# Kernel optimization log

Hardware: AMD Instinct MI355X
Metric: run time of the kernel (lower is better)

Reference implementation:

```python
import jax, jax.numpy as jnp
import numpy as np
from jax import lax

D_MODEL = 384
D_INNER = 768          # expand * d_model
D_HALF = D_INNER // 2  # 384
D_STATE = 16
D_CONV = 4
DT_RANK = 24           # ceil(384/16)
BATCH = 8
SEQLEN = 4097
EXTRAS = 1
LMAIN = SEQLEN - EXTRAS


def setup_inputs() -> dict:
    key = jax.random.key(0)
    ks = jax.random.split(key, 12)
    hidden_states = jax.random.normal(ks[0], (BATCH, SEQLEN, D_MODEL), jnp.float32)
    in_proj_w = jax.random.normal(ks[1], (D_INNER, D_MODEL), jnp.float32) * 0.02
    conv_x_w = jax.random.normal(ks[2], (D_HALF, 1, D_CONV), jnp.float32) * 0.2
    conv_z_w = jax.random.normal(ks[3], (D_HALF, 1, D_CONV), jnp.float32) * 0.2
    x_proj_w = jax.random.normal(ks[4], (DT_RANK + 2 * D_STATE, D_HALF), jnp.float32) * 0.02
    dt_std = DT_RANK ** -0.5
    dt_proj_w = jax.random.uniform(ks[5], (D_HALF, DT_RANK), jnp.float32, -dt_std, dt_std)
    # bias = inverse softplus of dt sampled log-uniform in [1e-3, 1e-1]
    dt = jnp.exp(jax.random.uniform(ks[6], (D_HALF,), jnp.float32)
                 * (jnp.log(0.1) - jnp.log(0.001)) + jnp.log(0.001))
    dt = jnp.clip(dt, 1e-4, None)
    dt_proj_b = dt + jnp.log(-jnp.expm1(-dt))
    A_log = jnp.log(jnp.broadcast_to(jnp.arange(1, D_STATE + 1, dtype=jnp.float32),
                                     (D_HALF, D_STATE)))
    D_param = jnp.ones((D_HALF,), jnp.float32)
    out_proj_w = jax.random.normal(ks[7], (D_MODEL, D_HALF), jnp.float32) * 0.02
    perm = jax.random.permutation(ks[8], LMAIN).astype(jnp.int64)
    perm_rev = jnp.argsort(perm).astype(jnp.int64)
    return {
        "hidden_states": hidden_states,
        "in_proj_w": in_proj_w,
        "conv_x_w": conv_x_w,
        "conv_z_w": conv_z_w,
        "x_proj_w": x_proj_w,
        "dt_proj_w": dt_proj_w,
        "dt_proj_b": dt_proj_b,
        "A_log": A_log,
        "D_param": D_param,
        "out_proj_w": out_proj_w,
        "perm": perm,
        "perm_rev": perm_rev,
    }


def _depthwise_conv_same(x, w):
    # x: (B, C, L), w: (C, 1, K); torch padding='same' for k=4 -> pad (left=1, right=2)
    total = D_CONV - 1
    left = total // 2
    return lax.conv_general_dilated(
        x, w, window_strides=(1,), padding=[(left, total - left)],
        dimension_numbers=("NCH", "OIH", "NCH"), feature_group_count=D_HALF)


def _selective_scan(x, dt, A, Bm, Cm, D_param, delta_bias):
    # x, dt: (B, d, L); A: (d, n); Bm, Cm: (B, n, L)
    dt = jax.nn.softplus(dt + delta_bias[None, :, None])
    xT = jnp.moveaxis(x, 2, 0)    # (L, B, d)
    dtT = jnp.moveaxis(dt, 2, 0)  # (L, B, d)
    BT = jnp.moveaxis(Bm, 2, 0)   # (L, B, n)
    CT = jnp.moveaxis(Cm, 2, 0)   # (L, B, n)

    def step(h, inp):
        x_t, dt_t, B_t, C_t = inp
        dA = jnp.exp(dt_t[..., None] * A)                      # (B, d, n)
        h = h * dA + (dt_t * x_t)[..., None] * B_t[:, None, :]  # (B, d, n)
        y = jnp.einsum("bdn,bn->bd", h, C_t)
        return h, y

    h0 = jnp.zeros((x.shape[0], x.shape[1], A.shape[1]), x.dtype)
    _, ys = lax.scan(step, h0, (xT, dtT, BT, CT))
    y = jnp.moveaxis(ys, 0, 2)  # (B, d, L)
    return y + D_param[None, :, None] * x


def reference(hidden_states, in_proj_w, conv_x_w, conv_z_w, x_proj_w,
              dt_proj_w, dt_proj_b, A_log, D_param, out_proj_w, perm, perm_rev):
    # in_proj (no bias): (B,L,D) -> (B, d_inner, L)
    xz = jnp.einsum("bld,ed->bel", hidden_states, in_proj_w)
    # hilbert/zigzag reorder on the main (non-extra) tokens
    xz = jnp.concatenate([xz[:, :, :EXTRAS], xz[:, :, EXTRAS:][:, :, perm]], axis=2)

    x, z = jnp.split(xz, 2, axis=1)  # (B, d_half, L) each
    A = -jnp.exp(A_log)
    x = jax.nn.silu(_depthwise_conv_same(x, conv_x_w))
    z = jax.nn.silu(_depthwise_conv_same(z, conv_z_w))

    x_dbl = jnp.einsum("bdl,ed->bel", x, x_proj_w)  # (B, dt_rank+2n, L)
    dt_low, Bm, Cm = jnp.split(x_dbl, [DT_RANK, DT_RANK + D_STATE], axis=1)
    dt = jnp.einsum("brl,dr->bdl", dt_low, dt_proj_w)

    y = _selective_scan(x, dt, A, Bm, Cm, D_param, dt_proj_b)
    y = (y * z).transpose(0, 2, 1)  # (B, L, d_half)
    out = jnp.einsum("bld,ed->ble", y, out_proj_w)  # (B, L, D)
    # undo the permutation on the output
    out = jnp.concatenate([out[:, :EXTRAS], out[:, EXTRAS:][:, perm_rev]], axis=1)
    return out
```

## Files before the change

kernel.cpp:

```cpp
#include <hip/hip_runtime.h>
#include <hip/hip_bf16.h>

#define DEVI __device__ __forceinline__

constexpr int B_   = 8;
constexpr int L_   = 4097;
constexpr int MTOT = B_ * L_;
constexpr int DH   = 384;
constexpr int NS   = 16;
constexpr int CH   = 33;
constexpr int NCH  = (L_ + CH - 1) / CH;

typedef __bf16 bf16x8 __attribute__((ext_vector_type(8)));
typedef float  f32x4  __attribute__((ext_vector_type(4)));

DEVI float bl(unsigned v) { return __uint_as_float(v << 16); }
DEVI float bh(unsigned v) { return __uint_as_float(v & 0xffff0000u); }
DEVI float bf(const __hip_bfloat16 x) { return __bfloat162float(x); }
DEVI unsigned short f2bu(float x) {
  __hip_bfloat16 b = __float2bfloat16(x);
  return *(unsigned short*)&b;
}
DEVI float u16f(const uint4& u, int j) {
  const unsigned w = (&u.x)[j >> 1];
  return (j & 1) ? bh(w) : bl(w);
}
DEVI float softplus_f(float x) {
  return (x > 20.f) ? x : __logf(1.f + __expf(x));
}

DEVI void gld16(const __hip_bfloat16* g, __hip_bfloat16* l) {
  __builtin_amdgcn_global_load_lds(
      (const __attribute__((address_space(1))) void*)g,
      (__attribute__((address_space(3))) void*)l, 16, 0, 0);
}

__global__ void flag_k(const void* hs, int* flagp) {
  if (threadIdx.x == 0 && blockIdx.x == 0) {
    const unsigned short* u = (const unsigned short*)hs;
    int ok = 1;
    for (int i = 0; i < 8; ++i) {
      const unsigned short v = u[2 * i];
      const int e = (v >> 7) & 0xFF;
      if (!(v == 0 || (e >= 100 && e <= 140))) ok = 0;
    }
    flagp[0] = ok;
    flagp[1] = 1;
  }
}

__global__ void a2prep_k(const void* __restrict__ alog, float* __restrict__ a2fo,
                         int* flagp) {
  const int d = threadIdx.x;
  const int f = flagp[0];
  float a2[16];
#pragma unroll
  for (int n = 0; n < 16; ++n) {
    const float v = f ? bf(((const __hip_bfloat16*)alog)[d * 16 + n])
                      : ((const float*)alog)[d * 16 + n];
    a2[n] = -1.4426950408889634f * __expf(v);
    a2fo[d * 16 + n] = a2[n];
  }
  int ok = 1;
#pragma unroll
  for (int n = 1; n < 16; ++n) {
    const float ref = (float)(n + 1) * a2[0];
    if (fabsf(a2[n] - ref) > 1e-3f * fabsf(ref)) ok = 0;
  }
  if (!ok) atomicAnd(&flagp[1], 0);
}

__global__ void perm_k(const int* p0, const int* p1, int* d0, int* d1) {
  __shared__ int s_or;
  const int* src = blockIdx.x ? p1 : p0;
  int*       dst = blockIdx.x ? d1 : d0;
  if (threadIdx.x == 0) s_or = 0;
  __syncthreads();
  int loc = 0;
  for (int i = threadIdx.x; i < 2048; i += 1024) loc |= src[2 * i + 1];
  atomicOr(&s_or, loc);
  __syncthreads();
  const bool is64 = (s_or == 0);
  for (int j = threadIdx.x; j < 4096; j += 1024)
    dst[j] = is64 ? (int)((const long long*)src)[j] : src[j];
}

struct NormSet { const void* src[8]; void* dst[8]; int n[8]; };
__global__ void norm_all(NormSet s, const int* flagp) {
  const int idx = blockIdx.x * 256 + threadIdx.x;
  const int f = flagp[0];
#pragma unroll
  for (int t = 0; t < 8; ++t) {
    if (idx < s.n[t]) {
      __hip_bfloat16* d = (__hip_bfloat16*)s.dst[t];
      if (f) d[idx] = ((const __hip_bfloat16*)s.src[t])[idx];
      else   d[idx] = __float2bfloat16(((const float*)s.src[t])[idx]);
    }
  }
}

__global__ void prep_k(const __hip_bfloat16* __restrict__ dtw,
                       const __hip_bfloat16* __restrict__ xw,
                       __hip_bfloat16* __restrict__ wcomb) {
  const int idx = blockIdx.x * 256 + threadIdx.x;
  if (idx >= 512 * 384) return;
  const int n = idx / 384, k = idx - n * 384;
  float v = 0.f;
  if (n < 384) {
#pragma unroll
    for (int r = 0; r < 24; ++r) v += bf(dtw[n * 24 + r]) * bf(xw[r * 384 + k]);
  } else if (n < 416) {
    v = bf(xw[(24 + n - 384) * 384 + k]);
  }
  wcomb[idx] = __float2bfloat16(v);
}

__global__ void cvt_k(const void* __restrict__ hs, __hip_bfloat16* __restrict__ dst,
                      const int* __restrict__ gidx, const int* __restrict__ flagp) {
  const int idx = blockIdx.x * 256 + threadIdx.x;
  if (idx >= MTOT * 48) return;
  const int j = idx % 48;
  const int r = idx / 48;
  const int b = r / L_, t = r - b * L_;
  const int src = b * L_ + (t == 0 ? 0 : 1 + gidx[t - 1]);
  uint4 o;
  if (flagp[0]) {
    o = *(const uint4*)((const __hip_bfloat16*)hs + (size_t)src * 384 + j * 8);
  } else {
    const float* f = (const float*)hs + (size_t)src * 384 + j * 8;
    const float4 f0 = *(const float4*)f;
    const float4 f1 = *(const float4*)(f + 4);
    o.x = f2bu(f0.x) | ((unsigned)f2bu(f0.y) << 16);
    o.y = f2bu(f0.z) | ((unsigned)f2bu(f0.w) << 16);
    o.z = f2bu(f1.x) | ((unsigned)f2bu(f1.y) << 16);
    o.w = f2bu(f1.z) | ((unsigned)f2bu(f1.w) << 16);
  }
  *(uint4*)(dst + (size_t)r * 384 + j * 8) = o;
}

template<int GATHER, int EPI>
__global__ __launch_bounds__(256, 3)
void gemm_k(const __hip_bfloat16* __restrict__ A, const __hip_bfloat16* __restrict__ W,
            void* __restrict__ e0, void* __restrict__ e1,
            const __hip_bfloat16* __restrict__ bias,
            const int* __restrict__ gidx, const int* __restrict__ flagp,
            int M, int N)
{
  __shared__ __align__(16) char smem[36864];
  __hip_bfloat16* lA = (__hip_bfloat16*)smem;
  __hip_bfloat16* lB = lA + 2 * 128 * 32;
  const int tid  = threadIdx.x;
  const int lane = tid & 63;
  const int wv   = tid >> 6;
  const int wm   = wv >> 1, wn = wv & 1;
  const int lrow = lane & 15, quad = lane >> 4;
  const int fbf  = flagp[0];

  const int NT = gridDim.x;
  const int nblocks = NT * (int)gridDim.y;
  const int id = blockIdx.y * NT + blockIdx.x;
  const int q8 = nblocks >> 3, r8 = nblocks & 7;
  const int xcd = id & 7, slot = id >> 3;
  const int nid = (xcd < r8 ? xcd * (q8 + 1)
                            : r8 * (q8 + 1) + (xcd - r8) * q8) + slot;
  const int mt = nid / NT, nt = nid - mt * NT;

  const bool live = !(EPI == 1 && nt * 128 + wn * 64 >= 416);

  const __hip_bfloat16* aSrc[4];
  const __hip_bfloat16* bSrc[4];
  __hip_bfloat16* aDst[4];
  __hip_bfloat16* bDst[4];
#pragma unroll
  for (int p = 0; p < 4; ++p) {
    const int s   = p * 256 + tid;
    const int kh  = s >> 9;
    const int row = (s >> 2) & 127;
    const int kc  = kh * 32 + (s & 3) * 8;
    int r = mt * 128 + row;
    if (r >= M) r = M - 1;
    int src;
    if (GATHER) { const int b = r / L_, t = r - b * L_;
                  src = b * L_ + (t == 0 ? 0 : 1 + gidx[t - 1]); }
    else        { src = r; }
    aSrc[p] = A + (size_t)src * 384 + kc;
    bSrc[p] = W + (size_t)(nt * 128 + row) * 384 + kc;
    aDst[p] = &lA[s * 8];
    bDst[p] = &lB[s * 8];
  }

  f32x4 acc[4][4] = {};

#pragma unroll
  for (int kt = 0; kt < 6; ++kt) {
    __syncthreads();
#pragma unroll
    for (int p = 0; p < 4; ++p) gld16(aSrc[p] + kt * 64, aDst[p]);
#pragma unroll
    for (int p = 0; p < 4; ++p) gld16(bSrc[p] + kt * 64, bDst[p]);
    __syncthreads();
    if (live) {
#pragma unroll
      for (int kh = 0; kh < 2; ++kh) {
        bf16x8 af[4], bfr[4];
#pragma unroll
        for (int i = 0; i < 4; ++i)
          af[i] = *reinterpret_cast<const bf16x8*>(
              &lA[kh * 4096 + (wm * 64 + i * 16 + lrow) * 32 + quad * 8]);
#pragma unroll
        for (int j = 0; j < 4; ++j)
          bfr[j] = *reinterpret_cast<const bf16x8*>(
              &lB[kh * 4096 + (wn * 64 + j * 16 + lrow) * 32 + quad * 8]);
#pragma unroll
        for (int i = 0; i < 4; ++i)
#pragma unroll
          for (int j = 0; j < 4; ++j)
            acc[i][j] = __builtin_amdgcn_mfma_f32_16x16x32_bf16(af[i], bfr[j], acc[i][j], 0, 0, 0);
      }
    }
  }

  const int r0c = mt * 128;
  if (EPI == 1 && nt == 3) {
#pragma unroll
    for (int i = 0; i < 4; ++i) {
      const int row0 = r0c + wm * 64 + i * 16 + quad * 4;
#pragma unroll
      for (int j = 0; j < 4; ++j) {
        const int col = 384 + wn * 64 + j * 16 + lrow;
        if (col >= 416) continue;
#pragma unroll
        for (int rg = 0; rg < 4; ++rg) {
          const int r = row0 + rg;
          if (r >= M) continue;
          ((float*)e1)[(size_t)r * 32 + (col - 384)] = acc[i][j][rg];
        }
      }
    }
  } else if (EPI == 2 && !fbf) {
    float* lT = (float*)smem;
#pragma unroll
    for (int h = 0; h < 2; ++h) {
      __syncthreads();
      if (wn == h) {
#pragma unroll
        for (int i = 0; i < 4; ++i)
#pragma unroll
          for (int j = 0; j < 4; ++j)
#pragma unroll
            for (int rg = 0; rg < 4; ++rg)
              lT[(wm * 64 + i * 16 + quad * 4 + rg) * 72 + j * 16 + lrow] = acc[i][j][rg];
      }
      __syncthreads();
#pragma unroll
      for (int p = 0; p < 8; ++p) {
        const int ch = p * 256 + tid;
        const int row = ch >> 4, c4 = (ch & 15) * 4;
        const int r = r0c + row;
        if (r < M) {
          const float4 v = *(const float4*)&lT[row * 72 + c4];
          *(float4*)((float*)e0 + (size_t)r * 384 + nt * 128 + h * 64 + c4) = v;
        }
      }
    }
  } else {
    __hip_bfloat16* lT = (__hip_bfloat16*)smem;
#pragma unroll
    for (int h = 0; h < 2; ++h) {
      __syncthreads();
      if (wn == h) {
        float bj[4] = {};
        if (EPI == 1) {
#pragma unroll
          for (int j = 0; j < 4; ++j)
            bj[j] = bf(bias[nt * 128 + h * 64 + j * 16 + lrow]);
        }
#pragma unroll
        for (int i = 0; i < 4; ++i)
#pragma unroll
          for (int j = 0; j < 4; ++j)
#pragma unroll
            for (int rg = 0; rg < 4; ++rg) {
              float v = acc[i][j][rg];
              if (EPI == 1) v = softplus_f(v + bj[j]);
              lT[(wm * 64 + i * 16 + quad * 4 + rg) * 72 + j * 16 + lrow] =
                  __float2bfloat16(v);
            }
      }
      __syncthreads();
#pragma unroll
      for (int p = 0; p < 4; ++p) {
        const int ch = p * 256 + tid;
        const int row = ch >> 3, c8 = (ch & 7) * 8;
        const int r = r0c + row;
        if (r < M) {
          const uint4 v = *(const uint4*)&lT[row * 72 + c8];
          const int g = nt * 128 + h * 64 + c8;
          __hip_bfloat16* dst = (EPI == 0 && g >= 384)
                ? (__hip_bfloat16*)e1 + (size_t)r * 384 + (g - 384)
                : (__hip_bfloat16*)e0 + (size_t)r * 384 + g;
          *(uint4*)dst = v;
        }
      }
    }
  }
}

__global__ void convx_k(const __hip_bfloat16* __restrict__ xh,
                        const __hip_bfloat16* __restrict__ cxw,
                        __hip_bfloat16* __restrict__ xc) {
  const int idx = blockIdx.x * 256 + threadIdx.x;
  if (idx >= MTOT * 48) return;
  const int g  = idx % 48;
  const int rg = idx / 48;
  const int t  = rg % L_;
  const int c0 = g * 8;
  uint4 wv[4];
#pragma unroll
  for (int p = 0; p < 4; ++p) wv[p] = *(const uint4*)(cxw + c0 * 4 + p * 8);
  float acc[8] = {};
#pragma unroll
  for (int k = 0; k < 4; ++k) {
    const int tt = t + k - 1;
    if (tt < 0 || tt >= L_) continue;
    const uint4 u = *(const uint4*)(xh + (size_t)(rg + k - 1) * 384 + c0);
#pragma unroll
    for (int j = 0; j < 8; ++j) {
      const int e = j * 4 + k;
      acc[j] += u16f(wv[e >> 3], e & 7) * u16f(u, j);
    }
  }
  uint4 o;
#pragma unroll
  for (int p = 0; p < 4; ++p) {
    const float s0 = acc[2 * p]     / (1.f + __expf(-acc[2 * p]));
    const float s1 = acc[2 * p + 1] / (1.f + __expf(-acc[2 * p + 1]));
    (&o.x)[p] = f2bu(s0) | ((unsigned)f2bu(s1) << 16);
  }
  *(uint4*)(xc + (size_t)rg * 384 + c0) = o;
}

__global__ __launch_bounds__(128)
void scan1_k(const __hip_bfloat16* __restrict__ dt, const float* __restrict__ bc,
             __hip_bfloat16* xcio,
             const float* __restrict__ a2f,
             const __hip_bfloat16* __restrict__ dpar,
             float* __restrict__ pbuf, float* __restrict__ hend,
             const int* __restrict__ flagp)
{
  __shared__ __align__(16) float lBC[CH * 32];
  const int blk = blockIdx.x;
  const int dt3 = blk % 3;
  const int c   = (blk / 3) % NCH;
  const int b   = blk / (3 * NCH);
  const int d   = dt3 * 128 + threadIdx.x;
  const int t0  = c * CH;
  const int r0  = b * L_ + t0;
  const int tmax = (L_ - t0 < CH) ? (L_ - t0) : CH;
  for (int i = threadIdx.x; i < tmax * 32; i += 128) lBC[i] = bc[(size_t)r0 * 32 + i];
  __syncthreads();

  float h[16];
#pragma unroll
  for (int n = 0; n < 16; ++n) h[n] = 0.f;
  float sdt = 0.f;
  const float Dd = bf(dpar[d]);
  const size_t base = ((size_t)(c * 8 + b) * 16) * 384 + d;

  if (flagp[1]) {
    const float a2b = a2f[d * 16];
    for (int tt = 0; tt < tmax; ++tt) {
      const size_t r = (size_t)(r0 + tt);
      const float dtv = bf(dt[r * 384 + d]);
      const float xv  = bf(xcio[r * 384 + d]);
      sdt += dtv;
      const float dtx = dtv * xv;
      float pw[17];
      pw[1] = exp2f(dtv * a2b);
#pragma unroll
      for (int n = 2; n <= 16; ++n) pw[n] = pw[n >> 1] * pw[n - (n >> 1)];
      float4 bq[4], cq[4];
#pragma unroll
      for (int q = 0; q < 4; ++q) {
        bq[q] = *(const float4*)&lBC[tt * 32 + q * 4];
        cq[q] = *(const float4*)&lBC[tt * 32 + 16 + q * 4];
      }
      float ya = 0.f, yb = 0.f;
#pragma unroll
      for (int n = 0; n < 16; ++n) {
        h[n] = h[n] * pw[n + 1] + dtx * (&bq[n >> 2].x)[n & 3];
        const float t = h[n] * (&cq[n >> 2].x)[n & 3];
        if (n & 1) yb += t; else ya += t;
      }
      const float y = ya + yb + Dd * xv;
      xcio[r * 384 + d] = __float2bfloat16(y);
    }
    float Ep[17];
    Ep[1] = exp2f(sdt * a2b);
#pragma unroll
    for (int n = 2; n <= 16; ++n) Ep[n] = Ep[n >> 1] * Ep[n - (n >> 1)];
#pragma unroll
    for (int n = 0; n < 16; ++n) {
      pbuf[base + n * 384] = Ep[n + 1];
      hend[base + n * 384] = h[n];
    }
  } else {
    float a2[16];
#pragma unroll
    for (int n = 0; n < 16; ++n) a2[n] = a2f[d * 16 + n];
    for (int tt = 0; tt < tmax; ++tt) {
      const size_t r = (size_t)(r0 + tt);
      const float dtv = bf(dt[r * 384 + d]);
      const float xv  = bf(xcio[r * 384 + d]);
      sdt += dtv;
      const float dtx = dtv * xv;
      float4 bq[4], cq[4];
#pragma unroll
      for (int q = 0; q < 4; ++q) {
        bq[q] = *(const float4*)&lBC[tt * 32 + q * 4];
        cq[q] = *(const float4*)&lBC[tt * 32 + 16 + q * 4];
      }
      float ya = 0.f, yb = 0.f;
#pragma unroll
      for (int n = 0; n < 16; ++n) {
        h[n] = h[n] * exp2f(dtv * a2[n]) + dtx * (&bq[n >> 2].x)[n & 3];
        const float t = h[n] * (&cq[n >> 2].x)[n & 3];
        if (n & 1) yb += t; else ya += t;
      }
      const float y = ya + yb + Dd * xv;
      xcio[r * 384 + d] = __float2bfloat16(y);
    }
#pragma unroll
    for (int n = 0; n < 16; ++n) {
      pbuf[base + n * 384] = exp2f(sdt * a2[n]);
      hend[base + n * 384] = h[n];
    }
  }
}

__global__ void scan2_k(float* __restrict__ pbuf, const float* __restrict__ hend) {
  const int tid = blockIdx.x * 256 + threadIdx.x;
  const int d = tid % 384;
  const int n = (tid / 384) & 15;
  const int b = tid / 6144;
  float H = 0.f;
  for (int c = 0; c < NCH; ++c) {
    const size_t idx = ((size_t)(c * 8 + b) * 16 + n) * 384 + d;
    const float p = pbuf[idx];
    const float he = hend[idx];
    pbuf[idx] = H;
    H = p * H + he;
  }
}

__global__ __launch_bounds__(128)
void scan3_k(__hip_bfloat16* dtyg, const float* __restrict__ bc,
             const __hip_bfloat16* __restrict__ yl,
             const __hip_bfloat16* __restrict__ zh,
             const __hip_bfloat16* __restrict__ czw,
             const float* __restrict__ a2f,
             const float* __restrict__ hstart,
             const int* __restrict__ flagp)
{
  __shared__ __align__(16) float lC[CH * 16];
  const int blk = blockIdx.x;
  const int dt3 = blk % 3;
  const int c   = (blk / 3) % NCH;
  const int b   = blk / (3 * NCH);
  const int d   = dt3 * 128 + threadIdx.x;
  const int t0  = c * CH;
  const int r0  = b * L_ + t0;
  const int tmax = (L_ - t0 < CH) ? (L_ - t0) : CH;
  for (int i = threadIdx.x; i < tmax * 16; i += 128)
    lC[i] = bc[(size_t)r0 * 32 + (i >> 4) * 32 + 16 + (i & 15)];
  __syncthreads();

  float hs_[16];
  const size_t base = ((size_t)(c * 8 + b) * 16) * 384 + d;
#pragma unroll
  for (int n = 0; n < 16; ++n) hs_[n] = hstart[base + n * 384];
  float cw[4];
#pragma unroll
  for (int k = 0; k < 4; ++k) cw[k] = bf(czw[d * 4 + k]);

  float zm1 = (t0 - 1 >= 0) ? bf(zh[(size_t)(r0 - 1) * 384 + d]) : 0.f;
  float z0  = bf(zh[(size_t)r0 * 384 + d]);
  float zp1 = (t0 + 1 < L_) ? bf(zh[(size_t)(r0 + 1) * 384 + d]) : 0.f;
  float sdt = 0.f;

  if (flagp[1]) {
    const float a2b = a2f[d * 16];
    for (int tt = 0; tt < tmax; ++tt) {
      const int t = t0 + tt;
      const size_t r = (size_t)(r0 + tt);
      const float zp2 = (t + 2 < L_) ? bf(zh[(r + 2) * 384 + d]) : 0.f;
      const float dtv = bf(dtyg[r * 384 + d]);
      sdt += dtv;
      float pw[17];
      pw[1] = exp2f(sdt * a2b);
#pragma unroll
      for (int n = 2; n <= 16; ++n) pw[n] = pw[n >> 1] * pw[n - (n >> 1)];
      float4 cq[4];
#pragma unroll
      for (int q = 0; q < 4; ++q) cq[q] = *(const float4*)&lC[tt * 16 + q * 4];
      float ca = 0.f, cb = 0.f;
#pragma unroll
      for (int n = 0; n < 16; ++n) {
        const float t2 = (&cq[n >> 2].x)[n & 3] * hs_[n] * pw[n + 1];
        if (n & 1) cb += t2; else ca += t2;
      }
      const float y = bf(yl[r * 384 + d]) + ca + cb;
      const float zc = cw[0] * zm1 + cw[1] * z0 + cw[2] * zp1 + cw[3] * zp2;
      const float zs = zc / (1.f + __expf(-zc));
      dtyg[r * 384 + d] = __float2bfloat16(y * zs);
      zm1 = z0; z0 = zp1; zp1 = zp2;
    }
  } else {
    float a2[16];
#pragma unroll
    for (int n = 0; n < 16; ++n) a2[n] = a2f[d * 16 + n];
    for (int tt = 0; tt < tmax; ++tt) {
      const int t = t0 + tt;
      const size_t r = (size_t)(r0 + tt);
      const float zp2 = (t + 2 < L_) ? bf(zh[(r + 2) * 384 + d]) : 0.f;
      const float dtv = bf(dtyg[r * 384 + d]);
      sdt += dtv;
      float4 cq[4];
#pragma unroll
      for (int q = 0; q < 4; ++q) cq[q] = *(const float4*)&lC[tt * 16 + q * 4];
      float ca = 0.f, cb = 0.f;
#pragma unroll
      for (int n = 0; n < 16; ++n) {
        const float t2 = (&cq[n >> 2].x)[n & 3] * hs_[n] * exp2f(sdt * a2[n]);
        if (n & 1) cb += t2; else ca += t2;
      }
      const float y = bf(yl[r * 384 + d]) + ca + cb;
      const float zc = cw[0] * zm1 + cw[1] * z0 + cw[2] * zp1 + cw[3] * zp2;
      const float zs = zc / (1.f + __expf(-zc));
      dtyg[r * 384 + d] = __float2bfloat16(y * zs);
      zm1 = z0; z0 = zp1; zp1 = zp2;
    }
  }
}

extern "C" void kernel_launch(void* const* d_in, const int* in_sizes, int n_in,
                              void* d_out, int out_size, void* d_ws, size_t ws_size,
                              hipStream_t stream) {
  const void* hs   = d_in[0];
  const void* w_in = d_in[1];
  const void* cxw  = d_in[2];
  const void* czw  = d_in[3];
  const void* xw   = d_in[4];
  const void* dtw  = d_in[5];
  const void* dtb  = d_in[6];
  const void* alog = d_in[7];
  const void* dpar = d_in[8];
  const void* ow   = d_in[9];
  const int* perm  = (const int*)d_in[10];
  const int* permr = (const int*)d_in[11];

  char* ws = (char*)d_ws;
  size_t off = 0;
  auto alloc = [&](size_t nbytes) -> char* {
    char* p = ws + off;
    off += (nbytes + 255) & ~(size_t)255;
    return p;
  };
  int* flag              = (int*)alloc(256);
  int* nperm             = (int*)alloc(4096 * 4);
  int* npermr            = (int*)alloc(4096 * 4);
  float* a2f             = (float*)alloc(6144 * 4);
  __hip_bfloat16* w_inb  = (__hip_bfloat16*)alloc(294912 * 2);
  __hip_bfloat16* cxwb   = (__hip_bfloat16*)alloc(1536 * 2);
  __hip_bfloat16* czwb   = (__hip_bfloat16*)alloc(1536 * 2);
  __hip_bfloat16* xwb    = (__hip_bfloat16*)alloc(21504 * 2);
  __hip_bfloat16* dtwb   = (__hip_bfloat16*)alloc(9216 * 2);
  __hip_bfloat16* dtbb   = (__hip_bfloat16*)alloc(384 * 2);
  __hip_bfloat16* dparb  = (__hip_bfloat16*)alloc(384 * 2);
  __hip_bfloat16* owb    = (__hip_bfloat16*)alloc(147456 * 2);
  __hip_bfloat16* wcombb = (__hip_bfloat16*)alloc((size_t)512 * 384 * 2);
  __hip_bfloat16* hsb    = (__hip_bfloat16*)alloc((size_t)MTOT * 384 * 2);
  __hip_bfloat16* zh     = (__hip_bfloat16*)alloc((size_t)MTOT * 384 * 2);
  __hip_bfloat16* xc     = (__hip_bfloat16*)alloc((size_t)MTOT * 384 * 2);
  __hip_bfloat16* dtyg   = (__hip_bfloat16*)alloc((size_t)MTOT * 384 * 2);
  float*          bcf    = (float*)alloc((size_t)MTOT * 32 * 4);
  __hip_bfloat16* xh   = (__hip_bfloat16*)d_out;
  float*          pbuf = (float*)d_out;
  float*          hend = (float*)((char*)d_out + (size_t)NCH * B_ * NS * DH * 4);

  flag_k<<<1, 64, 0, stream>>>(hs, flag);
  perm_k<<<2, 1024, 0, stream>>>(perm, permr, nperm, npermr);
  a2prep_k<<<1, 384, 0, stream>>>(alog, a2f, flag);
  NormSet ns;
  ns.src[0] = w_in; ns.dst[0] = w_inb; ns.n[0] = 294912;
  ns.src[1] = ow;   ns.dst[1] = owb;   ns.n[1] = 147456;
  ns.src[2] = xw;   ns.dst[2] = xwb;   ns.n[2] = 21504;
  ns.src[3] = dtw;  ns.dst[3] = dtwb;  ns.n[3] = 9216;
  ns.src[4] = cxw;  ns.dst[4] = cxwb;  ns.n[4] = 1536;
  ns.src[5] = czw;  ns.dst[5] = czwb;  ns.n[5] = 1536;
  ns.src[6] = dtb;  ns.dst[6] = dtbb;  ns.n[6] = 384;
  ns.src[7] = dpar; ns.dst[7] = dparb; ns.n[7] = 384;
  norm_all<<<1152, 256, 0, stream>>>(ns, flag);
  prep_k<<<768, 256, 0, stream>>>(dtwb, xwb, wcombb);
  cvt_k<<<(MTOT * 48 + 255) / 256, 256, 0, stream>>>(hs, hsb, nperm, flag);
  gemm_k<0, 0><<<dim3(6, 257), 256, 0, stream>>>(
      hsb, w_inb, xh, zh, nullptr, nullptr, flag, MTOT, 768);
  convx_k<<<(MTOT * 48 + 255) / 256, 256, 0, stream>>>(xh, cxwb, xc);
  gemm_k<0, 1><<<dim3(4, 257), 256, 0, stream>>>(
      xc, wcombb, dtyg, bcf, dtbb, nullptr, flag, MTOT, 512);
  scan1_k<<<B_ * NCH * 3, 128, 0, stream>>>(dtyg, bcf, xc, a2f, dparb, pbuf, hend, flag);
  scan2_k<<<192, 256, 0, stream>>>(pbuf, hend);
  scan3_k<<<B_ * NCH * 3, 128, 0, stream>>>(dtyg, bcf, xc, zh, czwb, a2f, pbuf, flag);
  gemm_k<1, 2><<<dim3(3, 257), 256, 0, stream>>>(
      dtyg, owb, d_out, nullptr, nullptr, npermr, flag, MTOT, 384);
  (void)in_sizes; (void)n_in; (void)out_size; (void)ws_size;
}
```

Before: 330.6 us.

## Restructure chunked scan: state-only first pass, recompute full recurrence from carried-in state

The first scan pass now only advances the hidden state over each chunk and stores the chunk's summed dt, no longer computing or writing per-token y. The prefix pass rebuilds each chunk's decay factor from the summed dt and A on the fly. The third pass reruns the full recurrence from the correct starting state, fusing the output and gating in one place. This removes the per-token y write and re-read and the stored decay buffer, at the cost of running the recurrence twice. Chunk size drops from 33 to 22, which gives more blocks but a longer sequential prefix pass.

```diff
diff --git a/kernel.cpp b/kernel.cpp
--- a/kernel.cpp
+++ b/kernel.cpp
@@ -8,7 +8,7 @@
 constexpr int MTOT = B_ * L_;
 constexpr int DH   = 384;
 constexpr int NS   = 16;
-constexpr int CH   = 33;
+constexpr int CH   = 22;
 constexpr int NCH  = (L_ + CH - 1) / CH;
 
 typedef __bf16 bf16x8 __attribute__((ext_vector_type(8)));
@@ -342,10 +342,98 @@
 
 __global__ __launch_bounds__(128)
 void scan1_k(const __hip_bfloat16* __restrict__ dt, const float* __restrict__ bc,
-             __hip_bfloat16* xcio,
+             const __hip_bfloat16* __restrict__ xc,
              const float* __restrict__ a2f,
+             float* __restrict__ sdtc, float* __restrict__ hend,
+             const int* __restrict__ flagp)
+{
+  __shared__ __align__(16) float lB[CH * 16];
+  const int blk = blockIdx.x;
+  const int dt3 = blk % 3;
+  const int c   = (blk / 3) % NCH;
+  const int b   = blk / (3 * NCH);
+  const int d   = dt3 * 128 + threadIdx.x;
+  const int t0  = c * CH;
+  const int r0  = b * L_ + t0;
+  const int tmax = (L_ - t0 < CH) ? (L_ - t0) : CH;
+  for (int i = threadIdx.x; i < tmax * 16; i += 128)
+    lB[i] = bc[(size_t)r0 * 32 + (i >> 4) * 32 + (i & 15)];
+  __syncthreads();
+
+  float h[16];
+#pragma unroll
+  for (int n = 0; n < 16; ++n) h[n] = 0.f;
+  float sdt = 0.f;
+  const size_t hbase = ((size_t)(c * 8 + b) * 16) * 384 + d;
+
+  if (flagp[1]) {
+    const float a2b = a2f[d * 16];
+    for (int tt = 0; tt < tmax; ++tt) {
+      const size_t r = (size_t)(r0 + tt);
+      const float dtv = bf(dt[r * 384 + d]);
+      const float xv  = bf(xc[r * 384 + d]);
+      sdt += dtv;
+      const float dtx = dtv * xv;
+      float pw[17];
+      pw[1] = exp2f(dtv * a2b);
+#pragma unroll
+      for (int n = 2; n <= 16; ++n) pw[n] = pw[n >> 1] * pw[n - (n >> 1)];
+      float4 bq[4];
+#pragma unroll
+      for (int q = 0; q < 4; ++q) bq[q] = *(const float4*)&lB[tt * 16 + q * 4];
+#pragma unroll
+      for (int n = 0; n < 16; ++n)
+        h[n] = h[n] * pw[n + 1] + dtx * (&bq[n >> 2].x)[n & 3];
+    }
+  } else {
+    float a2[16];
+#pragma unroll
+    for (int n = 0; n < 16; ++n) a2[n] = a2f[d * 16 + n];
+    for (int tt = 0; tt < tmax; ++tt) {
+      const size_t r = (size_t)(r0 + tt);
+      const float dtv = bf(dt[r * 384 + d]);
+      const float xv  = bf(xc[r * 384 + d]);
+      sdt += dtv;
+      const float dtx = dtv * xv;
+      float4 bq[4];
+#pragma unroll
+      for (int q = 0; q < 4; ++q) bq[q] = *(const float4*)&lB[tt * 16 + q * 4];
+#pragma unroll
+      for (int n = 0; n < 16; ++n)
+        h[n] = h[n] * exp2f(dtv * a2[n]) + dtx * (&bq[n >> 2].x)[n & 3];
+    }
+  }
+  sdtc[(size_t)(c * 8 + b) * 384 + d] = sdt;
+#pragma unroll
+  for (int n = 0; n < 16; ++n) hend[hbase + n * 384] = h[n];
+}
+
+__global__ void scan2_k(const float* __restrict__ sdtc, float* __restrict__ hh,
+                        const float* __restrict__ a2f) {
+  const int tid = blockIdx.x * 256 + threadIdx.x;
+  const int d = tid % 384;
+  const int n = (tid / 384) & 15;
+  const int b = tid / 6144;
+  const float a2n = a2f[d * 16 + n];
+  float H = 0.f;
+#pragma unroll 4
+  for (int c = 0; c < NCH; ++c) {
+    const size_t idx = ((size_t)(c * 8 + b) * 16 + n) * 384 + d;
+    const float sdt = sdtc[(size_t)(c * 8 + b) * 384 + d];
+    const float he = hh[idx];
+    hh[idx] = H;
+    H = exp2f(sdt * a2n) * H + he;
+  }
+}
+
+__global__ __launch_bounds__(128)
+void scan3_k(__hip_bfloat16* dtyg, const float* __restrict__ bc,
+             const __hip_bfloat16* __restrict__ xc,
+             const __hip_bfloat16* __restrict__ zh,
+             const __hip_bfloat16* __restrict__ czw,
              const __hip_bfloat16* __restrict__ dpar,
-             float* __restrict__ pbuf, float* __restrict__ hend,
+             const float* __restrict__ a2f,
+             const float* __restrict__ hstart,
              const int* __restrict__ flagp)
 {
   __shared__ __align__(16) float lBC[CH * 32];
@@ -361,124 +449,10 @@
   __syncthreads();
 
   float h[16];
-#pragma unroll
-  for (int n = 0; n < 16; ++n) h[n] = 0.f;
-  float sdt = 0.f;
+  const size_t hbase = ((size_t)(c * 8 + b) * 16) * 384 + d;
+#pragma unroll
+  for (int n = 0; n < 16; ++n) h[n] = hstart[hbase + n * 384];
   const float Dd = bf(dpar[d]);
-  const size_t base = ((size_t)(c * 8 + b) * 16) * 384 + d;
-
-  if (flagp[1]) {
-    const float a2b = a2f[d * 16];
-    for (int tt = 0; tt < tmax; ++tt) {
-      const size_t r = (size_t)(r0 + tt);
-      const float dtv = bf(dt[r * 384 + d]);
-      const float xv  = bf(xcio[r * 384 + d]);
-      sdt += dtv;
-      const float dtx = dtv * xv;
-      float pw[17];
-      pw[1] = exp2f(dtv * a2b);
-#pragma unroll
-      for (int n = 2; n <= 16; ++n) pw[n] = pw[n >> 1] * pw[n - (n >> 1)];
-      float4 bq[4], cq[4];
-#pragma unroll
-      for (int q = 0; q < 4; ++q) {
-        bq[q] = *(const float4*)&lBC[tt * 32 + q * 4];
-        cq[q] = *(const float4*)&lBC[tt * 32 + 16 + q * 4];
-      }
-      float ya = 0.f, yb = 0.f;
-#pragma unroll
-      for (int n = 0; n < 16; ++n) {
-        h[n] = h[n] * pw[n + 1] + dtx * (&bq[n >> 2].x)[n & 3];
-        const float t = h[n] * (&cq[n >> 2].x)[n & 3];
-        if (n & 1) yb += t; else ya += t;
-      }
-      const float y = ya + yb + Dd * xv;
-      xcio[r * 384 + d] = __float2bfloat16(y);
-    }
-    float Ep[17];
-    Ep[1] = exp2f(sdt * a2b);
-#pragma unroll
-    for (int n = 2; n <= 16; ++n) Ep[n] = Ep[n >> 1] * Ep[n - (n >> 1)];
-#pragma unroll
-    for (int n = 0; n < 16; ++n) {
-      pbuf[base + n * 384] = Ep[n + 1];
-      hend[base + n * 384] = h[n];
-    }
-  } else {
-    float a2[16];
-#pragma unroll
-    for (int n = 0; n < 16; ++n) a2[n] = a2f[d * 16 + n];
-    for (int tt = 0; tt < tmax; ++tt) {
-      const size_t r = (size_t)(r0 + tt);
-      const float dtv = bf(dt[r * 384 + d]);
-      const float xv  = bf(xcio[r * 384 + d]);
-      sdt += dtv;
-      const float dtx = dtv * xv;
-      float4 bq[4], cq[4];
-#pragma unroll
-      for (int q = 0; q < 4; ++q) {
-        bq[q] = *(const float4*)&lBC[tt * 32 + q * 4];
-        cq[q] = *(const float4*)&lBC[tt * 32 + 16 + q * 4];
-      }
-      float ya = 0.f, yb = 0.f;
-#pragma unroll
-      for (int n = 0; n < 16; ++n) {
-        h[n] = h[n] * exp2f(dtv * a2[n]) + dtx * (&bq[n >> 2].x)[n & 3];
-        const float t = h[n] * (&cq[n >> 2].x)[n & 3];
-        if (n & 1) yb += t; else ya += t;
-      }
-      const float y = ya + yb + Dd * xv;
-      xcio[r * 384 + d] = __float2bfloat16(y);
-    }
-#pragma unroll
-    for (int n = 0; n < 16; ++n) {
-      pbuf[base + n * 384] = exp2f(sdt * a2[n]);
-      hend[base + n * 384] = h[n];
-    }
-  }
-}
-
-__global__ void scan2_k(float* __restrict__ pbuf, const float* __restrict__ hend) {
-  const int tid = blockIdx.x * 256 + threadIdx.x;
-  const int d = tid % 384;
-  const int n = (tid / 384) & 15;
-  const int b = tid / 6144;
-  float H = 0.f;
-  for (int c = 0; c < NCH; ++c) {
-    const size_t idx = ((size_t)(c * 8 + b) * 16 + n) * 384 + d;
-    const float p = pbuf[idx];
-    const float he = hend[idx];
-    pbuf[idx] = H;
-    H = p * H + he;
-  }
-}
-
-__global__ __launch_bounds__(128)
-void scan3_k(__hip_bfloat16* dtyg, const float* __restrict__ bc,
-             const __hip_bfloat16* __restrict__ yl,
-             const __hip_bfloat16* __restrict__ zh,
-             const __hip_bfloat16* __restrict__ czw,
-             const float* __restrict__ a2f,
-             const float* __restrict__ hstart,
-             const int* __restrict__ flagp)
-{
-  __shared__ __align__(16) float lC[CH * 16];
-  const int blk = blockIdx.x;
-  const int dt3 = blk % 3;
-  const int c   = (blk / 3) % NCH;
-  const int b   = blk / (3 * NCH);
-  const int d   = dt3 * 128 + threadIdx.x;
-  const int t0  = c * CH;
-  const int r0  = b * L_ + t0;
-  const int tmax = (L_ - t0 < CH) ? (L_ - t0) : CH;
-  for (int i = threadIdx.x; i < tmax * 16; i += 128)
-    lC[i] = bc[(size_t)r0 * 32 + (i >> 4) * 32 + 16 + (i & 15)];
-  __syncthreads();
-
-  float hs_[16];
-  const size_t base = ((size_t)(c * 8 + b) * 16) * 384 + d;
-#pragma unroll
-  for (int n = 0; n < 16; ++n) hs_[n] = hstart[base + n * 384];
   float cw[4];
 #pragma unroll
   for (int k = 0; k < 4; ++k) cw[k] = bf(czw[d * 4 + k]);
@@ -486,7 +460,6 @@
   float zm1 = (t0 - 1 >= 0) ? bf(zh[(size_t)(r0 - 1) * 384 + d]) : 0.f;
   float z0  = bf(zh[(size_t)r0 * 384 + d]);
   float zp1 = (t0 + 1 < L_) ? bf(zh[(size_t)(r0 + 1) * 384 + d]) : 0.f;
-  float sdt = 0.f;
 
   if (flagp[1]) {
     const float a2b = a2f[d * 16];
@@ -495,21 +468,26 @@
       const size_t r = (size_t)(r0 + tt);
       const float zp2 = (t + 2 < L_) ? bf(zh[(r + 2) * 384 + d]) : 0.f;
       const float dtv = bf(dtyg[r * 384 + d]);
-      sdt += dtv;
+      const float xv  = bf(xc[r * 384 + d]);
+      const float dtx = dtv * xv;
       float pw[17];
-      pw[1] = exp2f(sdt * a2b);
+      pw[1] = exp2f(dtv * a2b);
 #pragma unroll
       for (int n = 2; n <= 16; ++n) pw[n] = pw[n >> 1] * pw[n - (n >> 1)];
-      float4 cq[4];
-#pragma unroll
-      for (int q = 0; q < 4; ++q) cq[q] = *(const float4*)&lC[tt * 16 + q * 4];
-      float ca = 0.f, cb = 0.f;
+      float4 bq[4], cq[4];
+#pragma unroll
+      for (int q = 0; q < 4; ++q) {
+        bq[q] = *(const float4*)&lBC[tt * 32 + q * 4];
+        cq[q] = *(const float4*)&lBC[tt * 32 + 16 + q * 4];
+      }
+      float ya = 0.f, yb = 0.f;
 #pragma unroll
       for (int n = 0; n < 16; ++n) {
-        const float t2 = (&cq[n >> 2].x)[n & 3] * hs_[n] * pw[n + 1];
-        if (n & 1) cb += t2; else ca += t2;
-      }
-      const float y = bf(yl[r * 384 + d]) + ca + cb;
+        h[n] = h[n] * pw[n + 1] + dtx * (&bq[n >> 2].x)[n & 3];
+        const float t2 = h[n] * (&cq[n >> 2].x)[n & 3];
+        if (n & 1) yb += t2; else ya += t2;
+      }
+      const float y = ya + yb + Dd * xv;
       const float zc = cw[0] * zm1 + cw[1] * z0 + cw[2] * zp1 + cw[3] * zp2;
       const float zs = zc / (1.f + __expf(-zc));
       dtyg[r * 384 + d] = __float2bfloat16(y * zs);
@@ -524,17 +502,22 @@
       const size_t r = (size_t)(r0 + tt);
       const float zp2 = (t + 2 < L_) ? bf(zh[(r + 2) * 384 + d]) : 0.f;
       const float dtv = bf(dtyg[r * 384 + d]);
-      sdt += dtv;
-      float4 cq[4];
-#pragma unroll
-      for (int q = 0; q < 4; ++q) cq[q] = *(const float4*)&lC[tt * 16 + q * 4];
-      float ca = 0.f, cb = 0.f;
+      const float xv  = bf(xc[r * 384 + d]);
+      const float dtx = dtv * xv;
+      float4 bq[4], cq[4];
+#pragma unroll
+      for (int q = 0; q < 4; ++q) {
+        bq[q] = *(const float4*)&lBC[tt * 32 + q * 4];
+        cq[q] = *(const float4*)&lBC[tt * 32 + 16 + q * 4];
+      }
+      float ya = 0.f, yb = 0.f;
 #pragma unroll
       for (int n = 0; n < 16; ++n) {
-        const float t2 = (&cq[n >> 2].x)[n & 3] * hs_[n] * exp2f(sdt * a2[n]);
-        if (n & 1) cb += t2; else ca += t2;
-      }
-      const float y = bf(yl[r * 384 + d]) + ca + cb;
+        h[n] = h[n] * exp2f(dtv * a2[n]) + dtx * (&bq[n >> 2].x)[n & 3];
+        const float t2 = h[n] * (&cq[n >> 2].x)[n & 3];
+        if (n & 1) yb += t2; else ya += t2;
+      }
+      const float y = ya + yb + Dd * xv;
       const float zc = cw[0] * zm1 + cw[1] * z0 + cw[2] * zp1 + cw[3] * zp2;
       const float zs = zc / (1.f + __expf(-zc));
       dtyg[r * 384 + d] = __float2bfloat16(y * zs);
@@ -585,8 +568,8 @@
   __hip_bfloat16* dtyg   = (__hip_bfloat16*)alloc((size_t)MTOT * 384 * 2);
   float*          bcf    = (float*)alloc((size_t)MTOT * 32 * 4);
   __hip_bfloat16* xh   = (__hip_bfloat16*)d_out;
-  float*          pbuf = (float*)d_out;
-  float*          hend = (float*)((char*)d_out + (size_t)NCH * B_ * NS * DH * 4);
+  float*          sdtc = (float*)d_out;
+  float*          hend = (float*)((char*)d_out + (size_t)NCH * B_ * DH * 4);
 
   flag_k<<<1, 64, 0, stream>>>(hs, flag);
   perm_k<<<2, 1024, 0, stream>>>(perm, permr, nperm, npermr);
@@ -608,9 +591,10 @@
   convx_k<<<(MTOT * 48 + 255) / 256, 256, 0, stream>>>(xh, cxwb, xc);
   gemm_k<0, 1><<<dim3(4, 257), 256, 0, stream>>>(
       xc, wcombb, dtyg, bcf, dtbb, nullptr, flag, MTOT, 512);
-  scan1_k<<<B_ * NCH * 3, 128, 0, stream>>>(dtyg, bcf, xc, a2f, dparb, pbuf, hend, flag);
-  scan2_k<<<192, 256, 0, stream>>>(pbuf, hend);
-  scan3_k<<<B_ * NCH * 3, 128, 0, stream>>>(dtyg, bcf, xc, zh, czwb, a2f, pbuf, flag);
+  scan1_k<<<B_ * NCH * 3, 128, 0, stream>>>(dtyg, bcf, xc, a2f, sdtc, hend, flag);
+  scan2_k<<<192, 256, 0, stream>>>(sdtc, hend, a2f);
+  scan3_k<<<B_ * NCH * 3, 128, 0, stream>>>(
+      dtyg, bcf, xc, zh, czwb, dparb, a2f, hend, flag);
   gemm_k<1, 2><<<dim3(3, 257), 256, 0, stream>>>(
       dtyg, owb, d_out, nullptr, nullptr, npermr, flag, MTOT, 384);
   (void)in_sizes; (void)n_in; (void)out_size; (void)ws_size;
```

Result: slower. 365.9 us (+10.7%).
